# Performance work log

Measured on AMD Instinct MI355X. Metric: run time of the kernel, lower is better.

## Reference

```python
import jax, jax.numpy as jnp
import numpy as np
import math

D_MODEL = 256
D_STATE = 64
B, L = 16, 4096
OUT_DIM = 2 * D_MODEL  # bidirectional


def s4d_kernel(log_dt, log_A_real, A_imag, C, L):
    # dt: [d], A: [d, n], C: [d, n, 2]
    dt = jnp.exp(log_dt)
    Cc = C[..., 0] + 1j * C[..., 1]
    A = -jnp.exp(log_A_real) + 1j * A_imag
    dtA = A * dt[:, None]                                   # [d, n]
    Cc = Cc * (jnp.exp(dtA) - 1.0) / (A + 1e-8)
    vand = jnp.exp(dtA[:, :, None] * jnp.arange(L))          # [d, n, L] complex
    K = 2.0 * jnp.einsum('dn,dnl->dl', Cc, vand).real        # [d, L]
    return K


def fft_conv(u, k, L):
    # u: [B, d, L], k: [d, L]; causal conv via zero-padded FFT
    kf = jnp.fft.rfft(k, n=2 * L)
    uf = jnp.fft.rfft(u, n=2 * L)
    return jnp.fft.irfft(uf * kf, n=2 * L)[..., :L]


def setup_inputs() -> dict:
    key = jax.random.key(0)
    ks = jax.random.split(key, 8)
    n = D_STATE // 2

    def kernel_params(k):
        log_dt = jnp.linspace(math.log(0.001), math.log(0.1), D_MODEL)
        log_A_real = jnp.tile(jnp.log(jnp.linspace(0.1, 0.9, n)), (D_MODEL, 1))
        A_imag = jnp.tile(jnp.linspace(0.0, math.pi, n), (D_MODEL, 1))
        C = jax.random.normal(k, (D_MODEL, n, 2)) / math.sqrt(D_STATE)
        return log_dt, log_A_real, A_imag, C

    log_dt_fw, log_A_real_fw, A_imag_fw, C_fw = kernel_params(ks[0])
    log_dt_bw, log_A_real_bw, A_imag_bw, C_bw = kernel_params(ks[1])

    return {
        'x': jax.random.normal(ks[2], (B, L, D_MODEL), dtype=jnp.float32),
        'log_dt_fw': log_dt_fw, 'log_A_real_fw': log_A_real_fw,
        'A_imag_fw': A_imag_fw, 'C_fw': C_fw,
        'log_dt_bw': log_dt_bw, 'log_A_real_bw': log_A_real_bw,
        'A_imag_bw': A_imag_bw, 'C_bw': C_bw,
        'Dskip': jax.random.normal(ks[3], (D_MODEL,)) * 0.01,
        'conv_w': jax.random.normal(ks[4], (2 * OUT_DIM, OUT_DIM)) / math.sqrt(OUT_DIM),
        'conv_b': jnp.zeros((2 * OUT_DIM,)),
        'ln_gamma': jnp.ones((OUT_DIM,)),
        'ln_beta': jnp.zeros((OUT_DIM,)),
    }


def reference(x, log_dt_fw, log_A_real_fw, A_imag_fw, C_fw,
              log_dt_bw, log_A_real_bw, A_imag_bw, C_bw,
              Dskip, conv_w, conv_b, ln_gamma, ln_beta):
    Bsz, Ln, H = x.shape
    u = jnp.swapaxes(x, 1, 2)                                # [B, H, L]

    k_fw = s4d_kernel(log_dt_fw, log_A_real_fw, A_imag_fw, C_fw, Ln)
    y_fw = fft_conv(u, k_fw, Ln) + u * Dskip[:, None]

    u_bw = jnp.flip(u, axis=-1)
    k_bw = s4d_kernel(log_dt_bw, log_A_real_bw, A_imag_bw, C_bw, Ln)
    y_bw = fft_conv(u_bw, k_bw, Ln) + u_bw * Dskip[:, None]
    y_bw = jnp.flip(y_bw, axis=-1)

    y = jnp.concatenate([y_fw, y_bw], axis=1)                # [B, 2H, L]
    y = jax.nn.gelu(y, approximate=False)
    # pointwise conv1d (kernel_size=1): channels 2H -> 4H
    y = jnp.einsum('oc,bcl->bol', conv_w, y) + conv_b[None, :, None]
    a, b = jnp.split(y, 2, axis=1)                           # GLU over channel dim
    y = a * jax.nn.sigmoid(b)                                # [B, 2H, L]
    y = jnp.swapaxes(y, 1, 2)                                # [B, L, 2H]
    # residual skipped: y.shape[-1] (2H) != x.shape[-1] (H)
    mu = jnp.mean(y, axis=-1, keepdims=True)
    var = jnp.var(y, axis=-1, keepdims=True)
    y = (y - mu) * jax.lax.rsqrt(var + 1e-5) * ln_gamma + ln_beta
    return y
```

## Files before the change

### kernel.cpp

```cpp
#include <hip/hip_runtime.h>
#include <hip/hip_bf16.h>
#include <cstdint>
#include <cstddef>

typedef __hip_bfloat16 bf16;
typedef __attribute__((ext_vector_type(8))) short short8;
typedef __attribute__((ext_vector_type(4))) float floatx4;
typedef __attribute__((ext_vector_type(16))) float floatx16;
typedef __attribute__((ext_vector_type(8))) _Float16 half8;

#define Bsz 16
#define Lseq 4096
#define Hd 256
#define NM 32
#define NCH 16
#define TCH 256
#define Mtot (Bsz*Lseq)

__device__ __forceinline__ float gelu_tanh(float y) {
  float y2 = y * y;
  float q = fmaf(0.044715f, y2, 1.0f);
  float a = 1.5957691216057308f * y * q;
  float e = __expf(-a);
  return y * __frcp_rn(1.0f + e);
}

__global__ __launch_bounds__(64) void k_prep(
    const float* __restrict__ ldt_fw, const float* __restrict__ lar_fw,
    const float* __restrict__ ai_fw,  const float* __restrict__ C_fw,
    const float* __restrict__ ldt_bw, const float* __restrict__ lar_bw,
    const float* __restrict__ ai_bw,  const float* __restrict__ C_bw,
    _Float16* __restrict__ Vm, _Float16* __restrict__ P,
    _Float16* __restrict__ KK, float* __restrict__ wtb) {
  const int d = blockIdx.x, dir = blockIdx.y;
  const int lane = threadIdx.x;
  const int n = lane & 31;
  const bool active = lane < 32;
  const float* ldt = dir ? ldt_bw : ldt_fw;
  const float* lar = dir ? lar_bw : lar_fw;
  const float* ai  = dir ? ai_bw  : ai_fw;
  const float* C   = dir ? C_bw   : C_fw;

  float dt = expf(ldt[d]);
  float Ar = -expf(lar[d * NM + n]);
  float Ai = ai[d * NM + n];
  float c0 = C[(d * NM + n) * 2 + 0];
  float c1 = C[(d * NM + n) * 2 + 1];

  float er = expf(Ar * dt);
  float sn, cs;
  sincosf(Ai * dt, &sn, &cs);
  float wr = er * cs, wi = er * sn;
  float nr = wr - 1.f, ni = wi;
  float tr_ = c0 * nr - c1 * ni;
  float ti  = c0 * ni + c1 * nr;
  float dr = Ar + 1e-8f, di = Ai;
  float inv = 1.f / (dr * dr + di * di);
  float Cr = 2.f * (tr_ * dr + ti * di) * inv;
  float Ci = 2.f * (ti * dr - tr_ * di) * inv;
  float erT = expf(256.f * Ar * dt);
  float snT, csT;
  sincosf(256.f * Ai * dt, &snT, &csT);
  if (active) {
    wtb[(dir * 256 + d) * 64 + 2 * n]     = erT * csT;
    wtb[(dir * 256 + d) * 64 + 2 * n + 1] = erT * snT;
  }
  _Float16* kk = KK + (dir * 256 + d) * 512;
  for (int i = lane; i < 512; i += 64) kk[i] = (_Float16)0.f;
  __syncthreads();

  _Float16* vm = Vm + (size_t)(dir * 256 + d) * 64 * 256;
  _Float16* pp = P  + (size_t)(dir * 256 + d) * 256 * 64;
  float pr = 1.f, pi = 0.f;
  for (int j = 0; j <= 256; ++j) {
    float kc = active ? (Cr * pr - Ci * pi) : 0.f;
#pragma unroll
    for (int off = 32; off > 0; off >>= 1) kc += __shfl_xor(kc, off);
    if (lane == 0 && j <= 255) {
      int i = dir ? (255 + j) : (255 - j);
      kk[i] = (_Float16)kc;
    }
    if (active) {
      if (j <= 255) {
        int tv = dir ? j : (255 - j);
        vm[(2 * n) * 256 + tv]     = (_Float16)pr;
        vm[(2 * n + 1) * 256 + tv] = (_Float16)pi;
      }
      if (j >= 1) {
        int t = dir ? (256 - j) : (j - 1);
        float cwr = Cr * pr - Ci * pi;
        float cwi = Cr * pi + Ci * pr;
        pp[t * 64 + 2 * n]     = (_Float16)cwr;
        pp[t * 64 + 2 * n + 1] = (_Float16)(-cwi);
      }
    }
    float npr = pr * wr - pi * wi;
    float npi = pr * wi + pi * wr;
    pr = npr; pi = npi;
  }
}

__global__ __launch_bounds__(256) void k_wconv(
    const float* __restrict__ W, bf16* __restrict__ Wb, int n) {
  int i = blockIdx.x * 256 + threadIdx.x;
  if (i < n) Wb[i] = __float2bfloat16(W[i]);
}

__global__ __launch_bounds__(256) void k_tr(
    const float* __restrict__ x, _Float16* __restrict__ x16) {
  __shared__ __align__(16) _Float16 t16[64][72];
  const int m0 = blockIdx.x * 64, d0 = blockIdx.y * 64;
  const int tid = threadIdx.x;
  {
    int li = tid >> 2, dq = (tid & 3) * 16;
    const float* src = x + (size_t)(m0 + li) * 256 + d0 + dq;
    float4 v0 = ((const float4*)src)[0];
    float4 v1 = ((const float4*)src)[1];
    float4 v2 = ((const float4*)src)[2];
    float4 v3 = ((const float4*)src)[3];
    half8 h0, h1;
    h0[0]=(_Float16)v0.x; h0[1]=(_Float16)v0.y; h0[2]=(_Float16)v0.z; h0[3]=(_Float16)v0.w;
    h0[4]=(_Float16)v1.x; h0[5]=(_Float16)v1.y; h0[6]=(_Float16)v1.z; h0[7]=(_Float16)v1.w;
    h1[0]=(_Float16)v2.x; h1[1]=(_Float16)v2.y; h1[2]=(_Float16)v2.z; h1[3]=(_Float16)v2.w;
    h1[4]=(_Float16)v3.x; h1[5]=(_Float16)v3.y; h1[6]=(_Float16)v3.z; h1[7]=(_Float16)v3.w;
    *(half8*)&t16[li][dq] = h0;
    *(half8*)&t16[li][dq + 8] = h1;
  }
  __syncthreads();
  {
    int dj = tid >> 2, lq = (tid & 3) * 16;
    half8 o0, o1;
#pragma unroll
    for (int i = 0; i < 8; ++i) {
      o0[i] = t16[lq + i][dj];
      o1[i] = t16[lq + 8 + i][dj];
    }
    _Float16* dst = x16 + (size_t)(d0 + dj) * 65536 + m0 + lq;
    ((half8*)dst)[0] = o0;
    ((half8*)dst)[1] = o1;
  }
}

__global__ __launch_bounds__(256) void k_mm1(
    const _Float16* __restrict__ x16, const _Float16* __restrict__ Vm,
    float* __restrict__ Sloc) {
  const int d = blockIdx.x, dir = blockIdx.y;
  const int tid = threadIdx.x, lane = tid & 63, wv = tid >> 6;
  __shared__ __align__(16) _Float16 ub[256][24];
  floatx16 acc[2][2];
#pragma unroll
  for (int a = 0; a < 2; ++a)
#pragma unroll
    for (int b = 0; b < 2; ++b)
#pragma unroll
      for (int i = 0; i < 16; ++i) acc[a][b][i] = 0.f;

  const _Float16* vmp = Vm + (size_t)(dir * 256 + d) * 64 * 256;
  const int arow = lane & 31, ak = (lane >> 5) * 8;
  const int colb = wv * 64;

  for (int ks = 0; ks < 16; ++ks) {
    const int tau0 = ks * 16;
    __syncthreads();
    {
      int col = tid;
      int b = col >> 4, c = col & 15;
      const _Float16* up = x16 + (size_t)d * 65536 + b * 4096 + c * 256 + tau0;
      ((int4*)&ub[col][0])[0] = ((const int4*)up)[0];
      ((int4*)&ub[col][0])[1] = ((const int4*)up)[1];
    }
    __syncthreads();
    half8 a0 = *(const half8*)(vmp + (size_t)(0 * 32 + arow) * 256 + tau0 + ak);
    half8 a1 = *(const half8*)(vmp + (size_t)(1 * 32 + arow) * 256 + tau0 + ak);
    half8 b0 = *(const half8*)&ub[colb + arow][ak];
    half8 b1 = *(const half8*)&ub[colb + 32 + arow][ak];
    acc[0][0] = __builtin_amdgcn_mfma_f32_32x32x16_f16(a0, b0, acc[0][0], 0, 0, 0);
    acc[0][1] = __builtin_amdgcn_mfma_f32_32x32x16_f16(a0, b1, acc[0][1], 0, 0, 0);
    acc[1][0] = __builtin_amdgcn_mfma_f32_32x32x16_f16(a1, b0, acc[1][0], 0, 0, 0);
    acc[1][1] = __builtin_amdgcn_mfma_f32_32x32x16_f16(a1, b1, acc[1][1], 0, 0, 0);
  }
  const int hi = lane >> 5;
#pragma unroll
  for (int rt = 0; rt < 2; ++rt)
#pragma unroll
    for (int ct = 0; ct < 2; ++ct) {
      int coll = colb + ct * 32 + (lane & 31);
      int b = coll >> 4, c = coll & 15;
      float* sp = Sloc + ((((size_t)(b * 2 + dir)) * 16 + c) * 256 + d) * 64;
#pragma unroll
      for (int r = 0; r < 16; r += 2) {
        int n2 = (r & 3) + 8 * (r >> 2) + 4 * hi + rt * 32;
        float2 v;
        v.x = acc[rt][ct][r];
        v.y = acc[rt][ct][r + 1];
        *(float2*)(sp + n2) = v;
      }
    }
}

__global__ __launch_bounds__(256) void k_scan2(
    const float* __restrict__ wtb, float* __restrict__ S) {
  const int b = blockIdx.x, dir = blockIdx.y;
  const int d = blockIdx.z * 64 + (threadIdx.x >> 2), h = threadIdx.x & 3;
  const int nbase = h * 8;
  float wTr[8], wTi[8], sr[8], si[8];
  const float* wt = wtb + (dir * 256 + d) * 64;
#pragma unroll
  for (int n = 0; n < 8; ++n) {
    wTr[n] = wt[2 * (nbase + n)];
    wTi[n] = wt[2 * (nbase + n) + 1];
    sr[n] = 0.f; si[n] = 0.f;
  }
  for (int cc = 0; cc < NCH; ++cc) {
    int c = dir ? (NCH - 1 - cc) : cc;
    float* p = S + ((((size_t)(b * 2 + dir)) * 16 + c) * 256 + d) * 64;
#pragma unroll
    for (int n = 0; n < 8; ++n) {
      int n2 = 2 * (nbase + n);
      float lr = p[n2], li = p[n2 + 1];
      p[n2] = sr[n]; p[n2 + 1] = si[n];
      float t0  = fmaf(wTr[n], sr[n], lr);
      float nsr = fmaf(-wTi[n], si[n], t0);
      float nsi = fmaf(wTr[n], si[n], li);
      nsi = fmaf(wTi[n], sr[n], nsi);
      sr[n] = nsr; si[n] = nsi;
    }
  }
}

__global__ __launch_bounds__(512) void k_mm2(
    const _Float16* __restrict__ x16, const _Float16* __restrict__ KK,
    const _Float16* __restrict__ P, const float* __restrict__ Sstart,
    const float* __restrict__ Dskip, bf16* __restrict__ ActT) {
  const int d = blockIdx.x, dir = blockIdx.y;
  const int tid = threadIdx.x, lane = tid & 63, wv = tid >> 6;
  __shared__ __align__(16) _Float16 ub[64][272];
  __shared__ __align__(16) _Float16 sb[64][72];
  __shared__ __align__(16) _Float16 kks[8][520];

  {
    const _Float16* kg = KK + (dir * 256 + d) * 512;
#pragma unroll
    for (int rr = 0; rr < 8; ++rr)
      for (int xx = tid; xx < 520; xx += 512) {
        int s = xx + rr;
        kks[rr][xx] = (s < 512) ? kg[s] : (_Float16)0.f;
      }
  }
  const float Dk = Dskip[d];
  const int t = wv * 32 + (lane & 31);
  const int hi = lane >> 5;
  const int r_sh = (255 - t) & 7;
  const _Float16* pp = P + (size_t)(dir * 256 + d) * 256 * 64 + (size_t)t * 64;

  for (int cb = 0; cb < 4; ++cb) {
    __syncthreads();
    {
      int col = tid >> 3, part = tid & 7;
      int coll = cb * 64 + col;
      int b = coll >> 4, c = coll & 15;
      const _Float16* up = x16 + (size_t)d * 65536 + b * 4096 + c * 256 + part * 32;
      ((int4*)&ub[col][part * 32])[0] = ((const int4*)up)[0];
      ((int4*)&ub[col][part * 32])[1] = ((const int4*)up)[1];
      ((int4*)&ub[col][part * 32])[2] = ((const int4*)up)[2];
      ((int4*)&ub[col][part * 32])[3] = ((const int4*)up)[3];
    }
    {
      int col = tid >> 3, part = tid & 7;
      int coll = cb * 64 + col;
      int b = coll >> 4, c = coll & 15;
      const float* sp = Sstart + ((((size_t)(b * 2 + dir)) * 16 + c) * 256 + d) * 64 + part * 8;
      float4 f0 = ((const float4*)sp)[0];
      float4 f1 = ((const float4*)sp)[1];
      half8 hv;
      hv[0]=(_Float16)f0.x; hv[1]=(_Float16)f0.y; hv[2]=(_Float16)f0.z; hv[3]=(_Float16)f0.w;
      hv[4]=(_Float16)f1.x; hv[5]=(_Float16)f1.y; hv[6]=(_Float16)f1.z; hv[7]=(_Float16)f1.w;
      *(half8*)&sb[col][part * 8] = hv;
    }
    __syncthreads();

    floatx16 acc0, acc1;
#pragma unroll
    for (int i = 0; i < 16; ++i) { acc0[i] = 0.f; acc1[i] = 0.f; }

#pragma unroll
    for (int ks = 0; ks < 16; ++ks) {
      int i0 = 255 - t + ks * 16 + hi * 8;
      half8 af = *(const half8*)&kks[r_sh][i0 - r_sh];
      half8 b0 = *(const half8*)&ub[(lane & 31)][ks * 16 + hi * 8];
      half8 b1 = *(const half8*)&ub[32 + (lane & 31)][ks * 16 + hi * 8];
      acc0 = __builtin_amdgcn_mfma_f32_32x32x16_f16(af, b0, acc0, 0, 0, 0);
      acc1 = __builtin_amdgcn_mfma_f32_32x32x16_f16(af, b1, acc1, 0, 0, 0);
    }
#pragma unroll
    for (int ks = 0; ks < 4; ++ks) {
      half8 af = *(const half8*)(pp + ks * 16 + hi * 8);
      half8 b0 = *(const half8*)&sb[(lane & 31)][ks * 16 + hi * 8];
      half8 b1 = *(const half8*)&sb[32 + (lane & 31)][ks * 16 + hi * 8];
      acc0 = __builtin_amdgcn_mfma_f32_32x32x16_f16(af, b0, acc0, 0, 0, 0);
      acc1 = __builtin_amdgcn_mfma_f32_32x32x16_f16(af, b1, acc1, 0, 0, 0);
    }
#pragma unroll
    for (int ct = 0; ct < 2; ++ct) {
      int coll = cb * 64 + ct * 32 + (lane & 31);
      int b = coll >> 4, c = coll & 15;
      bf16* op = ActT + (size_t)(dir * 256 + d) * 65536 + b * 4096 + c * 256;
      int ucol = ct * 32 + (lane & 31);
#pragma unroll
      for (int r = 0; r < 16; r += 2) {
        int tt = (r & 3) + 8 * (r >> 2) + 4 * hi + wv * 32;
        float a0 = (ct ? acc1[r] : acc0[r]);
        float a1 = (ct ? acc1[r + 1] : acc0[r + 1]);
        float u0 = (float)ub[ucol][tt];
        float u1 = (float)ub[ucol][tt + 1];
        float g0 = gelu_tanh(fmaf(u0, Dk, a0));
        float g1 = gelu_tanh(fmaf(u1, Dk, a1));
        bf16 h0 = __float2bfloat16(g0);
        bf16 h1 = __float2bfloat16(g1);
        unsigned pk = (unsigned)*(unsigned short*)&h0 |
                      ((unsigned)*(unsigned short*)&h1 << 16);
        *(unsigned*)(op + tt) = pk;
      }
    }
  }
}

__global__ __launch_bounds__(256) void k_tr2(
    const bf16* __restrict__ AT, bf16* __restrict__ A) {
  __shared__ __align__(16) short tl[64][72];
  const int m0 = blockIdx.x * 64, ch0 = blockIdx.y * 64;
  const int tid = threadIdx.x;
  {
    int chi = tid >> 2, mq = (tid & 3) * 16;
    const short* src = (const short*)AT + (size_t)(ch0 + chi) * 65536 + m0 + mq;
    *(int4*)&tl[chi][mq] = ((const int4*)src)[0];
    *(int4*)&tl[chi][mq + 8] = ((const int4*)src)[1];
  }
  __syncthreads();
  {
    int mi = tid >> 2, chq = (tid & 3) * 16;
    short8 s0, s1;
#pragma unroll
    for (int i = 0; i < 8; ++i) {
      s0[i] = tl[chq + i][mi];
      s1[i] = tl[chq + 8 + i][mi];
    }
    short* dst = (short*)A + (size_t)(m0 + mi) * 512 + ch0 + chq;
    ((short8*)dst)[0] = s0;
    ((short8*)dst)[1] = s1;
  }
}

#define LDK 40
__global__ __launch_bounds__(256) void k_gemm(
    const bf16* __restrict__ Act, const bf16* __restrict__ W,
    const float* __restrict__ bias, float* __restrict__ z) {
  __shared__ __align__(16) short As[128 * LDK];
  __shared__ __align__(16) short Bas[128 * LDK];
  __shared__ __align__(16) short Bgs[128 * LDK];
  const int bi = blockIdx.x, bj = blockIdx.y;
  const int tid = threadIdx.x, lane = tid & 63, wv = tid >> 6;
  const int wm = (wv & 1) * 64, wn = (wv >> 1) * 64;
  const int M0 = bi * 128;
  floatx4 acc_a[4][4], acc_g[4][4];
#pragma unroll
  for (int i = 0; i < 4; ++i)
#pragma unroll
    for (int j = 0; j < 4; ++j) {
      acc_a[i][j] = (floatx4){0.f, 0.f, 0.f, 0.f};
      acc_g[i][j] = (floatx4){0.f, 0.f, 0.f, 0.f};
    }
  const int row2 = tid >> 2;
  const int kc = (tid & 3) * 8;
  const int fr = lane & 15, fk = (lane >> 4) * 8;

  for (int kb = 0; kb < 512; kb += 32) {
#pragma unroll
    for (int r = 0; r < 2; ++r) {
      int rr = row2 + r * 64;
      *(int4*)&As[rr * LDK + kc]  = *(const int4*)&Act[(size_t)(M0 + rr) * 512 + kb + kc];
      *(int4*)&Bas[rr * LDK + kc] = *(const int4*)&W[(size_t)(bj * 128 + rr) * 512 + kb + kc];
      *(int4*)&Bgs[rr * LDK + kc] = *(const int4*)&W[(size_t)(512 + bj * 128 + rr) * 512 + kb + kc];
    }
    __syncthreads();
    short8 af[4], bfa[4], bfg[4];
#pragma unroll
    for (int i = 0; i < 4; ++i) af[i]  = *(const short8*)&As[(wm + 16 * i + fr) * LDK + fk];
#pragma unroll
    for (int j = 0; j < 4; ++j) bfa[j] = *(const short8*)&Bas[(wn + 16 * j + fr) * LDK + fk];
#pragma unroll
    for (int j = 0; j < 4; ++j) bfg[j] = *(const short8*)&Bgs[(wn + 16 * j + fr) * LDK + fk];
#pragma unroll
    for (int i = 0; i < 4; ++i)
#pragma unroll
      for (int j = 0; j < 4; ++j) {
        acc_a[i][j] = __builtin_amdgcn_mfma_f32_16x16x32_bf16(af[i], bfa[j], acc_a[i][j], 0, 0, 0);
        acc_g[i][j] = __builtin_amdgcn_mfma_f32_16x16x32_bf16(af[i], bfg[j], acc_g[i][j], 0, 0, 0);
      }
    __syncthreads();
  }
  const int col = lane & 15, rquad = (lane >> 4) * 4;
#pragma unroll
  for (int j = 0; j < 4; ++j) {
    int o = bj * 128 + wn + 16 * j + col;
    float ba = bias[o];
    float bg = bias[512 + o];
#pragma unroll
    for (int i = 0; i < 4; ++i) {
      int mbase = M0 + wm + 16 * i + rquad;
#pragma unroll
      for (int rg = 0; rg < 4; ++rg) {
        float a = acc_a[i][j][rg] + ba;
        float g = acc_g[i][j][rg] + bg;
        float zv = a * __frcp_rn(1.f + __expf(-g));
        z[(size_t)(mbase + rg) * 512 + o] = zv;
      }
    }
  }
}

__global__ __launch_bounds__(256) void k_ln(
    float* __restrict__ z, const float* __restrict__ gamma,
    const float* __restrict__ beta) {
  const int m = blockIdx.x * 4 + (threadIdx.x >> 6);
  const int lane = threadIdx.x & 63;
  float* zp = z + (size_t)m * 512;
  float v[8], s = 0.f, sq = 0.f;
#pragma unroll
  for (int j = 0; j < 8; ++j) {
    v[j] = zp[j * 64 + lane];
    s += v[j];
    sq = fmaf(v[j], v[j], sq);
  }
#pragma unroll
  for (int off = 32; off > 0; off >>= 1) {
    s += __shfl_xor(s, off);
    sq += __shfl_xor(sq, off);
  }
  float mean = s * (1.f / 512.f);
  float var = fmaf(-mean, mean, sq * (1.f / 512.f));
  float inv = rsqrtf(var + 1e-5f);
#pragma unroll
  for (int j = 0; j < 8; ++j) {
    int cidx = j * 64 + lane;
    float g = gamma[cidx], be = beta[cidx];
    zp[cidx] = fmaf((v[j] - mean) * inv, g, be);
  }
}

extern "C" void kernel_launch(void* const* d_in, const int* in_sizes, int n_in,
                              void* d_out, int out_size, void* d_ws, size_t ws_size,
                              hipStream_t stream) {
  const float* x      = (const float*)d_in[0];
  const float* ldt_fw = (const float*)d_in[1];
  const float* lar_fw = (const float*)d_in[2];
  const float* ai_fw  = (const float*)d_in[3];
  const float* C_fw   = (const float*)d_in[4];
  const float* ldt_bw = (const float*)d_in[5];
  const float* lar_bw = (const float*)d_in[6];
  const float* ai_bw  = (const float*)d_in[7];
  const float* C_bw   = (const float*)d_in[8];
  const float* Dskip  = (const float*)d_in[9];
  const float* W      = (const float*)d_in[10];
  const float* bias   = (const float*)d_in[11];
  const float* gamma  = (const float*)d_in[12];
  const float* beta   = (const float*)d_in[13];
  float* out = (float*)d_out;

  char* wsb = (char*)d_ws;
  bf16*     ActT  = (bf16*)wsb;
  float*    SlocT = (float*)(wsb + 67108864u);
  _Float16* x16   = (_Float16*)(wsb + 100663296u);
  _Float16* Vm    = (_Float16*)(wsb + 134217728u);
  _Float16* P     = (_Float16*)(wsb + 150994944u);
  _Float16* KK    = (_Float16*)(wsb + 167772160u);
  float*    wtb   = (float*)(wsb + 168296448u);
  bf16*     Wb    = (bf16*)(wsb + 168427520u);
  bf16*     Act   = (bf16*)(wsb + 67108864u);

  k_prep<<<dim3(256, 2), dim3(64), 0, stream>>>(
      ldt_fw, lar_fw, ai_fw, C_fw, ldt_bw, lar_bw, ai_bw, C_bw, Vm, P, KK, wtb);
  k_wconv<<<dim3(2048), dim3(256), 0, stream>>>(W, Wb, 1024 * 512);
  k_tr<<<dim3(Mtot / 64, 4), dim3(256), 0, stream>>>(x, x16);
  k_mm1<<<dim3(256, 2), dim3(256), 0, stream>>>(x16, Vm, SlocT);
  k_scan2<<<dim3(Bsz, 2, 4), dim3(256), 0, stream>>>(wtb, SlocT);
  k_mm2<<<dim3(256, 2), dim3(512), 0, stream>>>(x16, KK, P, SlocT, Dskip, ActT);
  k_tr2<<<dim3(Mtot / 64, 8), dim3(256), 0, stream>>>(ActT, Act);
  k_gemm<<<dim3(Mtot / 128, 4), dim3(256), 0, stream>>>(Act, Wb, bias, out);
  k_ln<<<dim3(Mtot / 4), dim3(256), 0, stream>>>(out, gamma, beta);
}
```

Before: 637.4 us.

## Shrink GLU GEMM N-tile, prefetch next K-slice into registers, reorder grid

The GLU GEMM now computes 64 output columns per block instead of 128, which halves the accumulators and B-tile shared memory, and it requests three blocks per CU through launch bounds. The global loads for the next K-slice are issued before the MFMAs and written to shared memory after the second barrier, so load latency overlaps compute. The grid is reordered so blocks sharing the same M rows run next to each other, which should help L2 reuse of the activation tile. In exchange the activation tile is reloaded by twice as many blocks, and arithmetic intensity per block is lower.

Result: faster. 532.0 us (-16.5%).

```diff
diff --git a/kernel.cpp b/kernel.cpp
--- a/kernel.cpp
+++ b/kernel.cpp
@@ -352,21 +352,21 @@
 }
 
 #define LDK 40
-__global__ __launch_bounds__(256) void k_gemm(
+__global__ __launch_bounds__(256, 3) void k_gemm(
     const bf16* __restrict__ Act, const bf16* __restrict__ W,
     const float* __restrict__ bias, float* __restrict__ z) {
   __shared__ __align__(16) short As[128 * LDK];
-  __shared__ __align__(16) short Bas[128 * LDK];
-  __shared__ __align__(16) short Bgs[128 * LDK];
-  const int bi = blockIdx.x, bj = blockIdx.y;
+  __shared__ __align__(16) short Bas[64 * LDK];
+  __shared__ __align__(16) short Bgs[64 * LDK];
+  const int nj = blockIdx.x, bi = blockIdx.y;
   const int tid = threadIdx.x, lane = tid & 63, wv = tid >> 6;
-  const int wm = (wv & 1) * 64, wn = (wv >> 1) * 64;
-  const int M0 = bi * 128;
-  floatx4 acc_a[4][4], acc_g[4][4];
+  const int wm = (wv & 1) * 64, wn = (wv >> 1) * 32;
+  const int M0 = bi * 128, N0 = nj * 64;
+  floatx4 acc_a[4][2], acc_g[4][2];
 #pragma unroll
   for (int i = 0; i < 4; ++i)
 #pragma unroll
-    for (int j = 0; j < 4; ++j) {
+    for (int j = 0; j < 2; ++j) {
       acc_a[i][j] = (floatx4){0.f, 0.f, 0.f, 0.f};
       acc_g[i][j] = (floatx4){0.f, 0.f, 0.f, 0.f};
     }
@@ -374,35 +374,52 @@
   const int kc = (tid & 3) * 8;
   const int fr = lane & 15, fk = (lane >> 4) * 8;
 
+  const bf16* pa0 = Act + (size_t)(M0 + row2) * 512 + kc;
+  const bf16* pa1 = Act + (size_t)(M0 + row2 + 64) * 512 + kc;
+  const bf16* pba = W + (size_t)(N0 + row2) * 512 + kc;
+  const bf16* pbg = W + (size_t)(512 + N0 + row2) * 512 + kc;
+
+  *(int4*)&As[row2 * LDK + kc]        = *(const int4*)pa0;
+  *(int4*)&As[(row2 + 64) * LDK + kc] = *(const int4*)pa1;
+  *(int4*)&Bas[row2 * LDK + kc]       = *(const int4*)pba;
+  *(int4*)&Bgs[row2 * LDK + kc]       = *(const int4*)pbg;
+
   for (int kb = 0; kb < 512; kb += 32) {
-#pragma unroll
-    for (int r = 0; r < 2; ++r) {
-      int rr = row2 + r * 64;
-      *(int4*)&As[rr * LDK + kc]  = *(const int4*)&Act[(size_t)(M0 + rr) * 512 + kb + kc];
-      *(int4*)&Bas[rr * LDK + kc] = *(const int4*)&W[(size_t)(bj * 128 + rr) * 512 + kb + kc];
-      *(int4*)&Bgs[rr * LDK + kc] = *(const int4*)&W[(size_t)(512 + bj * 128 + rr) * 512 + kb + kc];
-    }
     __syncthreads();
-    short8 af[4], bfa[4], bfg[4];
+    short8 af[4], bfa[2], bfg[2];
 #pragma unroll
     for (int i = 0; i < 4; ++i) af[i]  = *(const short8*)&As[(wm + 16 * i + fr) * LDK + fk];
 #pragma unroll
-    for (int j = 0; j < 4; ++j) bfa[j] = *(const short8*)&Bas[(wn + 16 * j + fr) * LDK + fk];
-#pragma unroll
-    for (int j = 0; j < 4; ++j) bfg[j] = *(const short8*)&Bgs[(wn + 16 * j + fr) * LDK + fk];
+    for (int j = 0; j < 2; ++j) bfa[j] = *(const short8*)&Bas[(wn + 16 * j + fr) * LDK + fk];
+#pragma unroll
+    for (int j = 0; j < 2; ++j) bfg[j] = *(const short8*)&Bgs[(wn + 16 * j + fr) * LDK + fk];
+    int4 ga0, ga1, gb, gg;
+    const bool more = (kb + 32) < 512;
+    if (more) {
+      ga0 = *(const int4*)(pa0 + kb + 32);
+      ga1 = *(const int4*)(pa1 + kb + 32);
+      gb  = *(const int4*)(pba + kb + 32);
+      gg  = *(const int4*)(pbg + kb + 32);
+    }
 #pragma unroll
     for (int i = 0; i < 4; ++i)
 #pragma unroll
-      for (int j = 0; j < 4; ++j) {
+      for (int j = 0; j < 2; ++j) {
         acc_a[i][j] = __builtin_amdgcn_mfma_f32_16x16x32_bf16(af[i], bfa[j], acc_a[i][j], 0, 0, 0);
         acc_g[i][j] = __builtin_amdgcn_mfma_f32_16x16x32_bf16(af[i], bfg[j], acc_g[i][j], 0, 0, 0);
       }
     __syncthreads();
+    if (more) {
+      *(int4*)&As[row2 * LDK + kc]        = ga0;
+      *(int4*)&As[(row2 + 64) * LDK + kc] = ga1;
+      *(int4*)&Bas[row2 * LDK + kc]       = gb;
+      *(int4*)&Bgs[row2 * LDK + kc]       = gg;
+    }
   }
   const int col = lane & 15, rquad = (lane >> 4) * 4;
 #pragma unroll
-  for (int j = 0; j < 4; ++j) {
-    int o = bj * 128 + wn + 16 * j + col;
+  for (int j = 0; j < 2; ++j) {
+    int o = N0 + wn + 16 * j + col;
     float ba = bias[o];
     float bg = bias[512 + o];
 #pragma unroll
@@ -486,6 +503,6 @@
   k_scan2<<<dim3(Bsz, 2, 4), dim3(256), 0, stream>>>(wtb, SlocT);
   k_mm2<<<dim3(256, 2), dim3(512), 0, stream>>>(x16, KK, P, SlocT, Dskip, ActT);
   k_tr2<<<dim3(Mtot / 64, 8), dim3(256), 0, stream>>>(ActT, Act);
-  k_gemm<<<dim3(Mtot / 128, 4), dim3(256), 0, stream>>>(Act, Wb, bias, out);
+  k_gemm<<<dim3(8, Mtot / 128), dim3(256), 0, stream>>>(Act, Wb, bias, out);
   k_ln<<<dim3(Mtot / 4), dim3(256), 0, stream>>>(out, gamma, beta);
 }
```
